# Optimization experiments

Hardware: AMD Instinct MI355X
Metric: run time of the kernel (lower is better)

The kernel has to match this reference:

```python
import jax, jax.numpy as jnp
import numpy as np

N_SRC = 50000
N_DST = 50000
E = 800000
F_IN = 128
H = 4
D = 32
NEG_SLOPE = 0.2


def setup_inputs() -> dict:
    key = jax.random.key(0)
    k1, k2, k3, k4, k5, k6, k7, k8 = jax.random.split(key, 8)
    src_feat = jax.random.normal(k1, (N_SRC, F_IN), dtype=jnp.float32)
    dst_feat = jax.random.normal(k2, (N_DST, F_IN), dtype=jnp.float32)
    edge_feat = jax.random.normal(k3, (E, F_IN), dtype=jnp.float32)
    src_idx = jax.random.randint(k4, (E,), 0, N_SRC, dtype=jnp.int32)
    dst_idx = jax.random.randint(k5, (E,), 0, N_DST, dtype=jnp.int32)
    # fc_src: in = 2*F_IN (concat op), out = H*D; fc_dst: in = F_IN, out = H*D
    g = np.sqrt(2.0)  # gain for 'relu' (xavier_normal_)
    W_src = jax.random.normal(k6, (2 * F_IN, H * D), dtype=jnp.float32) * (g * np.sqrt(2.0 / (2 * F_IN + H * D)))
    W_dst = jax.random.normal(k7, (F_IN, H * D), dtype=jnp.float32) * (g * np.sqrt(2.0 / (F_IN + H * D)))
    bias = jnp.zeros((H * D,), dtype=jnp.float32)
    return {"src_feat": src_feat, "dst_feat": dst_feat, "edge_feat": edge_feat,
            "W_src": W_src, "W_dst": W_dst, "bias": bias,
            "src_idx": src_idx, "dst_idx": dst_idx}


def reference(src_feat, dst_feat, edge_feat, W_src, W_dst, bias, src_idx, dst_idx):
    # Per-edge message: concat(src[e], edge[e]) @ W_src -> [E, H, D]
    m = jnp.concatenate([src_feat[src_idx], edge_feat], axis=1) @ W_src
    m = m.reshape(E, H, D)
    # Destination projection: [N_dst, H, D]
    nh = (dst_feat @ W_dst).reshape(N_DST, H, D)
    # e_add_v then LeakyReLU -> attention logits [E, H, D]
    scores = jax.nn.leaky_relu(m + nh[dst_idx], negative_slope=NEG_SLOPE)
    # edge_softmax: segment softmax over edges incident to each destination,
    # computed independently per (head, out_feat) channel.
    mx = jax.ops.segment_max(scores, dst_idx, num_segments=N_DST)
    ex = jnp.exp(scores - mx[dst_idx])
    denom = jax.ops.segment_sum(ex, dst_idx, num_segments=N_DST)
    attn = ex / denom[dst_idx]
    # Weighted scatter-add aggregation -> [N_dst, H, D]
    rst = jax.ops.segment_sum(m * attn, dst_idx, num_segments=N_DST)
    rst = rst + bias.reshape(1, H, D)
    return rst
```

## Files before the change

### kernel.cpp

```cpp
#include <hip/hip_runtime.h>


#define F 128
#define C 128
#define NEG 0.2f
#define NN 50000
#define EE 800000

typedef _Float16 half8 __attribute__((ext_vector_type(8)));
typedef float f32x4 __attribute__((ext_vector_type(4)));

__device__ __forceinline__ void fma4(float4& a, float s, const float4 w) {
    a.x += s * w.x; a.y += s * w.y; a.z += s * w.z; a.w += s * w.w;
}

__global__ __launch_bounds__(256) void node_proj_kernel(
    const float* __restrict__ src_feat, const float* __restrict__ dst_feat,
    const float* __restrict__ W_src, const float* __restrict__ W_dst,
    float* __restrict__ src_proj, float* __restrict__ nh)
{
    const float* in; const float* W; float* out;
    if (blockIdx.y == 0) { in = src_feat; W = W_src; out = src_proj; }
    else                 { in = dst_feat; W = W_dst; out = nh; }

    __shared__ float4 xs[8 * 32];
    const int t  = threadIdx.x;
    const int nb = blockIdx.x * 8;

    {
        int row = t >> 5, col = t & 31;
        xs[t] = ((const float4*)(in + (size_t)(nb + row) * F))[col];
    }
    __syncthreads();

    const int jq = t & 31;
    const int ng = t >> 5;
    float4 acc = make_float4(0.f, 0.f, 0.f, 0.f);
    const float4* W4 = (const float4*)W;

    #pragma unroll 4
    for (int k4 = 0; k4 < 32; ++k4) {
        float4 xv = xs[ng * 32 + k4];
        float4 w0 = W4[(4 * k4 + 0) * 32 + jq];
        float4 w1 = W4[(4 * k4 + 1) * 32 + jq];
        float4 w2 = W4[(4 * k4 + 2) * 32 + jq];
        float4 w3 = W4[(4 * k4 + 3) * 32 + jq];
        fma4(acc, xv.x, w0); fma4(acc, xv.y, w1);
        fma4(acc, xv.z, w2); fma4(acc, xv.w, w3);
    }
    ((float4*)(out + (size_t)(nb + ng) * C))[jq] = acc;
}

__global__ __launch_bounds__(256) void hist_kernel(
    const int* __restrict__ dst_idx, int* __restrict__ deg)
{
    int e = blockIdx.x * 256 + threadIdx.x;
    if (e < EE) atomicAdd(&deg[dst_idx[e]], 1);
}

__global__ __launch_bounds__(1024) void scan_kernel(
    const int* __restrict__ deg, int* __restrict__ cursor)
{
    __shared__ int ssum[1024];
    const int t = threadIdx.x;
    const int chunk = (NN + 1023) / 1024;
    int lo = t * chunk, hi = lo + chunk; if (hi > NN) hi = NN; if (lo > NN) lo = NN;
    int s = 0;
    for (int i = lo; i < hi; ++i) s += deg[i];
    ssum[t] = s;
    __syncthreads();
    for (int d = 1; d < 1024; d <<= 1) {
        int v = (t >= d) ? ssum[t - d] : 0;
        __syncthreads();
        ssum[t] += v;
        __syncthreads();
    }
    int run = ssum[t] - s;
    for (int i = lo; i < hi; ++i) { cursor[i] = run; run += deg[i]; }
}

__global__ __launch_bounds__(256) void scatter_kernel(
    const int* __restrict__ dst_idx, int* __restrict__ cursor, int* __restrict__ elist)
{
    int e = blockIdx.x * 256 + threadIdx.x;
    if (e < EE) {
        int p = atomicAdd(&cursor[dst_idx[e]], 1);
        elist[p] = e;
    }
}

__global__ __launch_bounds__(256) void prep_w_kernel(
    const float* __restrict__ W_src, _Float16* __restrict__ bfrag)
{
    int i = blockIdx.x * 256 + threadIdx.x;
    int j  = i & 7;
    int lw = (i >> 3) & 63;
    int ks = (i >> 9) & 3;
    int ct = i >> 11;
    int k  = ks * 32 + (lw >> 4) * 8 + j;
    int ch = ct * 16 + (lw & 15);
    bfrag[i] = (_Float16)W_src[(size_t)(128 + k) * 128 + ch];
}

__global__ __launch_bounds__(256) void edge_kernel(
    const float* __restrict__ edge_feat, const _Float16* __restrict__ bfrag,
    const float* __restrict__ src_proj, const float* __restrict__ nh,
    const int* __restrict__ src_idx, const int* __restrict__ dst_idx,
    const int* __restrict__ elist,
    float* __restrict__ num, float* __restrict__ den)
{
    const int t   = threadIdx.x;
    const int l   = t & 63;
    const int w   = t >> 6;
    const int ebw = (blockIdx.x * 4 + w) * 16;
    const int er  = l & 15;
    const int g   = l >> 4;

    int e_reg = 0, s_reg = 0, d_reg = 0;
    if (l < 16) {
        e_reg = elist[ebw + l];
        s_reg = src_idx[e_reg];
        d_reg = dst_idx[e_reg];
    }

    const float4* rp = (const float4*)(edge_feat + (size_t)__shfl(e_reg, er) * F);
    const half8*  B  = (const half8*)bfrag;

    f32x4 acc[8];
    #pragma unroll
    for (int ct = 0; ct < 8; ++ct) acc[ct] = (f32x4){0.f, 0.f, 0.f, 0.f};

    #pragma unroll
    for (int ks = 0; ks < 4; ++ks) {
        float4 f0 = rp[ks * 8 + g * 2];
        float4 f1 = rp[ks * 8 + g * 2 + 1];
        half8 a;
        a[0] = (_Float16)f0.x; a[1] = (_Float16)f0.y;
        a[2] = (_Float16)f0.z; a[3] = (_Float16)f0.w;
        a[4] = (_Float16)f1.x; a[5] = (_Float16)f1.y;
        a[6] = (_Float16)f1.z; a[7] = (_Float16)f1.w;
        #pragma unroll
        for (int ct = 0; ct < 8; ++ct) {
            half8 b = B[(ct * 4 + ks) * 64 + l];
            acc[ct] = __builtin_amdgcn_mfma_f32_16x16x32_f16(a, b, acc[ct], 0, 0, 0);
        }
    }

    int cur = __shfl(d_reg, g * 4);
    float nv[8], nacc[8], dacc[8];
    #pragma unroll
    for (int ct = 0; ct < 8; ++ct) {
        nv[ct]   = nh[(size_t)cur * C + ct * 16 + er];
        nacc[ct] = 0.f;
        dacc[ct] = 0.f;
    }

    #pragma unroll
    for (int rg = 0; rg < 4; ++rg) {
        const int el  = g * 4 + rg;
        const int d   = __shfl(d_reg, el);
        const int sid = __shfl(s_reg, el);
        if (d != cur) {
            #pragma unroll
            for (int ct = 0; ct < 8; ++ct) {
                atomicAdd(num + (size_t)cur * C + ct * 16 + er, nacc[ct]);
                atomicAdd(den + (size_t)cur * C + ct * 16 + er, dacc[ct]);
                nacc[ct] = 0.f;
                dacc[ct] = 0.f;
            }
            cur = d;
            #pragma unroll
            for (int ct = 0; ct < 8; ++ct) nv[ct] = nh[(size_t)cur * C + ct * 16 + er];
        }
        const float* sprow = src_proj + (size_t)sid * C + er;
        #pragma unroll
        for (int ct = 0; ct < 8; ++ct) {
            float m = acc[ct][rg] + sprow[ct * 16];
            float s = m + nv[ct];
            s = s > 0.f ? s : NEG * s;
            float ex = __expf(s);
            nacc[ct] += ex * m;
            dacc[ct] += ex;
        }
    }
    #pragma unroll
    for (int ct = 0; ct < 8; ++ct) {
        atomicAdd(num + (size_t)cur * C + ct * 16 + er, nacc[ct]);
        atomicAdd(den + (size_t)cur * C + ct * 16 + er, dacc[ct]);
    }
}

__global__ __launch_bounds__(256) void finalize_kernel(
    const float* __restrict__ num, const float* __restrict__ den,
    const float* __restrict__ bias, float* __restrict__ out)
{
    int i = blockIdx.x * 256 + threadIdx.x;
    float4 n = ((const float4*)num)[i];
    float4 d = ((const float4*)den)[i];
    float4 b = ((const float4*)bias)[i & 31];
    float4 r;
    r.x = (d.x != 0.f ? n.x / d.x : 0.f) + b.x;
    r.y = (d.y != 0.f ? n.y / d.y : 0.f) + b.y;
    r.z = (d.z != 0.f ? n.z / d.z : 0.f) + b.z;
    r.w = (d.w != 0.f ? n.w / d.w : 0.f) + b.w;
    ((float4*)out)[i] = r;
}

extern "C" void kernel_launch(void* const* d_in, const int* in_sizes, int n_in,
                              void* d_out, int out_size, void* d_ws, size_t ws_size,
                              hipStream_t stream) {
    const float* src_feat  = (const float*)d_in[0];
    const float* dst_feat  = (const float*)d_in[1];
    const float* edge_feat = (const float*)d_in[2];
    const float* W_src     = (const float*)d_in[3];
    const float* W_dst     = (const float*)d_in[4];
    const float* bias      = (const float*)d_in[5];
    const int*   src_idx   = (const int*)d_in[6];
    const int*   dst_idx   = (const int*)d_in[7];
    float* out = (float*)d_out;

    const size_t NODEF = (size_t)NN * C;

    float* ws       = (float*)d_ws;
    float* src_proj = ws;
    float* nh       = ws + NODEF;
    float* den      = ws + 2 * NODEF;
    int*   deg      = (int*)(ws + 3 * NODEF);
    int*   cursor   = deg + NN;
    int*   elist    = cursor + NN;
    _Float16* bfrag = (_Float16*)(elist + EE);

    float* num = out;

    hipMemsetAsync(num, 0, NODEF * sizeof(float), stream);
    hipMemsetAsync(den, 0, NODEF * sizeof(float), stream);
    hipMemsetAsync(deg, 0, NN * sizeof(int), stream);

    hist_kernel<<<(EE + 255) / 256, 256, 0, stream>>>(dst_idx, deg);
    scan_kernel<<<1, 1024, 0, stream>>>(deg, cursor);
    scatter_kernel<<<(EE + 255) / 256, 256, 0, stream>>>(dst_idx, cursor, elist);

    prep_w_kernel<<<64, 256, 0, stream>>>(W_src, bfrag);

    node_proj_kernel<<<dim3(NN / 8, 2), 256, 0, stream>>>(
        src_feat, dst_feat, W_src, W_dst, src_proj, nh);

    edge_kernel<<<EE / 64, 256, 0, stream>>>(
        edge_feat, bfrag, src_proj, nh, src_idx, dst_idx, elist, num, den);

    finalize_kernel<<<NODEF / 4 / 256, 256, 0, stream>>>(num, den, bias, out);
}
```

Measured before the change: 1.448 ms.

## Tile node projection in LDS, parallelize degree scan, stage MFMA weights in LDS

Node projection now processes 32 rows per block with the weight matrix staged in shared memory in two halves, so each thread reuses every weight load across 4 rows. The single-block serial-chunk scan becomes a three-kernel multi-block scan. The edge kernel prefetches its edge-feature rows into registers and copies the fp16 weight fragments into LDS before the MFMA loop. These target global-memory weight traffic and the serial scan latency. In exchange they add extra launches and larger LDS use, which may lower occupancy.

```diff
diff --git a/kernel.cpp b/kernel.cpp
--- a/kernel.cpp
+++ b/kernel.cpp
@@ -6,6 +6,7 @@
 #define NEG 0.2f
 #define NN 50000
 #define EE 800000
+#define SCAN_NB 49
 
 typedef _Float16 half8 __attribute__((ext_vector_type(8)));
 typedef float f32x4 __attribute__((ext_vector_type(4)));
@@ -23,32 +24,55 @@
     if (blockIdx.y == 0) { in = src_feat; W = W_src; out = src_proj; }
     else                 { in = dst_feat; W = W_dst; out = nh; }
 
-    __shared__ float4 xs[8 * 32];
+    __shared__ float4 Wl[2048];
+    __shared__ float4 xs[1024];
     const int t  = threadIdx.x;
-    const int nb = blockIdx.x * 8;
-
-    {
-        int row = t >> 5, col = t & 31;
-        xs[t] = ((const float4*)(in + (size_t)(nb + row) * F))[col];
-    }
-    __syncthreads();
+    const int nb = blockIdx.x * 32;
+
+    #pragma unroll
+    for (int i = 0; i < 4; ++i) {
+        int flat = i * 256 + t;
+        int row = flat >> 5, col = flat & 31;
+        xs[flat] = (nb + row < NN)
+                 ? ((const float4*)(in + (size_t)(nb + row) * F))[col]
+                 : make_float4(0.f, 0.f, 0.f, 0.f);
+    }
 
     const int jq = t & 31;
-    const int ng = t >> 5;
-    float4 acc = make_float4(0.f, 0.f, 0.f, 0.f);
-    const float4* W4 = (const float4*)W;
-
-    #pragma unroll 4
-    for (int k4 = 0; k4 < 32; ++k4) {
-        float4 xv = xs[ng * 32 + k4];
-        float4 w0 = W4[(4 * k4 + 0) * 32 + jq];
-        float4 w1 = W4[(4 * k4 + 1) * 32 + jq];
-        float4 w2 = W4[(4 * k4 + 2) * 32 + jq];
-        float4 w3 = W4[(4 * k4 + 3) * 32 + jq];
-        fma4(acc, xv.x, w0); fma4(acc, xv.y, w1);
-        fma4(acc, xv.z, w2); fma4(acc, xv.w, w3);
-    }
-    ((float4*)(out + (size_t)(nb + ng) * C))[jq] = acc;
+    const int rg = t >> 5;
+    float4 acc[4];
+    #pragma unroll
+    for (int rr = 0; rr < 4; ++rr) acc[rr] = make_float4(0.f, 0.f, 0.f, 0.f);
+
+    const float4* Wg = (const float4*)W;
+
+    #pragma unroll
+    for (int half = 0; half < 2; ++half) {
+        __syncthreads();
+        #pragma unroll
+        for (int i = 0; i < 8; ++i) Wl[i * 256 + t] = Wg[half * 2048 + i * 256 + t];
+        __syncthreads();
+
+        #pragma unroll 2
+        for (int k4 = 0; k4 < 16; ++k4) {
+            float4 w0 = Wl[(4 * k4 + 0) * 32 + jq];
+            float4 w1 = Wl[(4 * k4 + 1) * 32 + jq];
+            float4 w2 = Wl[(4 * k4 + 2) * 32 + jq];
+            float4 w3 = Wl[(4 * k4 + 3) * 32 + jq];
+            #pragma unroll
+            for (int rr = 0; rr < 4; ++rr) {
+                float4 xv = xs[(rg * 4 + rr) * 32 + half * 16 + k4];
+                fma4(acc[rr], xv.x, w0); fma4(acc[rr], xv.y, w1);
+                fma4(acc[rr], xv.z, w2); fma4(acc[rr], xv.w, w3);
+            }
+        }
+    }
+
+    #pragma unroll
+    for (int rr = 0; rr < 4; ++rr) {
+        int row = nb + rg * 4 + rr;
+        if (row < NN) ((float4*)(out + (size_t)row * C))[jq] = acc[rr];
+    }
 }
 
 __global__ __launch_bounds__(256) void hist_kernel(
@@ -58,25 +82,44 @@
     if (e < EE) atomicAdd(&deg[dst_idx[e]], 1);
 }
 
-__global__ __launch_bounds__(1024) void scan_kernel(
-    const int* __restrict__ deg, int* __restrict__ cursor)
-{
-    __shared__ int ssum[1024];
+__global__ __launch_bounds__(1024) void scan_a_kernel(
+    const int* __restrict__ deg, int* __restrict__ cursor, int* __restrict__ bsum)
+{
+    __shared__ int s[1024];
     const int t = threadIdx.x;
-    const int chunk = (NN + 1023) / 1024;
-    int lo = t * chunk, hi = lo + chunk; if (hi > NN) hi = NN; if (lo > NN) lo = NN;
-    int s = 0;
-    for (int i = lo; i < hi; ++i) s += deg[i];
-    ssum[t] = s;
+    const int i = blockIdx.x * 1024 + t;
+    int v = (i < NN) ? deg[i] : 0;
+    s[t] = v;
     __syncthreads();
     for (int d = 1; d < 1024; d <<= 1) {
-        int v = (t >= d) ? ssum[t - d] : 0;
+        int u = (t >= d) ? s[t - d] : 0;
         __syncthreads();
-        ssum[t] += v;
+        s[t] += u;
         __syncthreads();
     }
-    int run = ssum[t] - s;
-    for (int i = lo; i < hi; ++i) { cursor[i] = run; run += deg[i]; }
+    if (i < NN) cursor[i] = s[t] - v;
+    if (t == 1023) bsum[blockIdx.x] = s[t];
+}
+
+__global__ __launch_bounds__(64) void scan_b_kernel(
+    const int* __restrict__ bsum, int* __restrict__ boff)
+{
+    const int t = threadIdx.x;
+    int v = (t < SCAN_NB) ? bsum[t] : 0;
+    int incl = v;
+    #pragma unroll
+    for (int d = 1; d < 64; d <<= 1) {
+        int u = __shfl_up(incl, d);
+        if (t >= d) incl += u;
+    }
+    if (t < SCAN_NB) boff[t] = incl - v;
+}
+
+__global__ __launch_bounds__(1024) void scan_c_kernel(
+    int* __restrict__ cursor, const int* __restrict__ boff)
+{
+    const int i = blockIdx.x * 1024 + threadIdx.x;
+    if (i < NN) cursor[i] += boff[blockIdx.x];
 }
 
 __global__ __launch_bounds__(256) void scatter_kernel(
@@ -109,6 +152,8 @@
     const int* __restrict__ elist,
     float* __restrict__ num, float* __restrict__ den)
 {
+    __shared__ __align__(16) half8 Blds[2048];
+
     const int t   = threadIdx.x;
     const int l   = t & 63;
     const int w   = t >> 6;
@@ -124,7 +169,20 @@
     }
 
     const float4* rp = (const float4*)(edge_feat + (size_t)__shfl(e_reg, er) * F);
-    const half8*  B  = (const half8*)bfrag;
+    float4 fA[8];
+    #pragma unroll
+    for (int ks = 0; ks < 4; ++ks) {
+        fA[2 * ks]     = rp[ks * 8 + g * 2];
+        fA[2 * ks + 1] = rp[ks * 8 + g * 2 + 1];
+    }
+
+    {
+        const float4* bg = (const float4*)bfrag;
+        float4* bl = (float4*)Blds;
+        #pragma unroll
+        for (int i = 0; i < 8; ++i) bl[i * 256 + t] = bg[i * 256 + t];
+    }
+    __syncthreads();
 
     f32x4 acc[8];
     #pragma unroll
@@ -132,8 +190,7 @@
 
     #pragma unroll
     for (int ks = 0; ks < 4; ++ks) {
-        float4 f0 = rp[ks * 8 + g * 2];
-        float4 f1 = rp[ks * 8 + g * 2 + 1];
+        float4 f0 = fA[2 * ks], f1 = fA[2 * ks + 1];
         half8 a;
         a[0] = (_Float16)f0.x; a[1] = (_Float16)f0.y;
         a[2] = (_Float16)f0.z; a[3] = (_Float16)f0.w;
@@ -141,7 +198,7 @@
         a[6] = (_Float16)f1.z; a[7] = (_Float16)f1.w;
         #pragma unroll
         for (int ct = 0; ct < 8; ++ct) {
-            half8 b = B[(ct * 4 + ks) * 64 + l];
+            half8 b = Blds[(ct * 4 + ks) * 64 + l];
             acc[ct] = __builtin_amdgcn_mfma_f32_16x16x32_f16(a, b, acc[ct], 0, 0, 0);
         }
     }
@@ -229,6 +286,8 @@
     int*   cursor   = deg + NN;
     int*   elist    = cursor + NN;
     _Float16* bfrag = (_Float16*)(elist + EE);
+    int*   bsum     = (int*)(bfrag + 16384);
+    int*   boff     = bsum + 64;
 
     float* num = out;
 
@@ -237,12 +296,14 @@
     hipMemsetAsync(deg, 0, NN * sizeof(int), stream);
 
     hist_kernel<<<(EE + 255) / 256, 256, 0, stream>>>(dst_idx, deg);
-    scan_kernel<<<1, 1024, 0, stream>>>(deg, cursor);
+    scan_a_kernel<<<SCAN_NB, 1024, 0, stream>>>(deg, cursor, bsum);
+    scan_b_kernel<<<1, 64, 0, stream>>>(bsum, boff);
+    scan_c_kernel<<<SCAN_NB, 1024, 0, stream>>>(cursor, boff);
     scatter_kernel<<<(EE + 255) / 256, 256, 0, stream>>>(dst_idx, cursor, elist);
 
     prep_w_kernel<<<64, 256, 0, stream>>>(W_src, bfrag);
 
-    node_proj_kernel<<<dim3(NN / 8, 2), 256, 0, stream>>>(
+    node_proj_kernel<<<dim3((NN + 31) / 32, 2), 256, 0, stream>>>(
         src_feat, dst_feat, W_src, W_dst, src_proj, nh);
 
     edge_kernel<<<EE / 64, 256, 0, stream>>>(
```

Measured after the change: 1.245 ms. 14.0% less time.
